# Optimization experiments

Hardware: AMD Instinct MI355X
Metric: run time of the kernel (lower is better)

## Reference

```python
import jax, jax.numpy as jnp
import numpy as np

B, Z, H, TC, TD, DOUT = 128, 512, 512, 16, 16, 176
DIN_DEC = DOUT + H  # 688: concat(prev_note, conductor_embedding)


def setup_inputs() -> dict:
    key = jax.random.key(0)
    ks = jax.random.split(key, 24)

    def glorot(k, shape):
        lim = np.sqrt(6.0 / (shape[0] + shape[1]))
        return jax.random.uniform(k, shape, jnp.float32, -lim, lim)

    return {
        'z_ssm_embedding': jax.random.normal(ks[0], (B, Z), jnp.float32),
        'pianoroll': jax.random.uniform(ks[1], (B, TC * TD, DOUT), jnp.float32),
        'ssm': jax.random.uniform(ks[2], (B, TC * TD, TC * TD), jnp.float32),
        # z -> conductor initial states (h1,c1,h2,c2), tanh dense
        'Wz': glorot(ks[3], (Z, 4 * H)), 'bz': jnp.zeros((4 * H,), jnp.float32),
        # conductor 2-layer LSTM (input 512)
        'cond_W1': glorot(ks[4], (H, 4 * H)), 'cond_U1': glorot(ks[5], (H, 4 * H)), 'cond_b1': jnp.zeros((4 * H,), jnp.float32),
        'cond_W2': glorot(ks[6], (H, 4 * H)), 'cond_U2': glorot(ks[7], (H, 4 * H)), 'cond_b2': jnp.zeros((4 * H,), jnp.float32),
        # conductor embedding -> decoder initial states, tanh dense
        'Wcd': glorot(ks[8], (H, 4 * H)), 'bcd': jnp.zeros((4 * H,), jnp.float32),
        # core decoder 2-layer LSTM (input 688)
        'dec_W1': glorot(ks[9], (DIN_DEC, 4 * H)), 'dec_U1': glorot(ks[10], (H, 4 * H)), 'dec_b1': jnp.zeros((4 * H,), jnp.float32),
        'dec_W2': glorot(ks[11], (H, 4 * H)), 'dec_U2': glorot(ks[12], (H, 4 * H)), 'dec_b2': jnp.zeros((4 * H,), jnp.float32),
        # output projection (softmax)
        'Wp': glorot(ks[13], (H, DOUT)), 'bp': jnp.zeros((DOUT,), jnp.float32),
    }


def _lstm_step(x, h, c, W, U, b):
    g = x @ W + h @ U + b  # (B, 4H), keras gate order i,f,g,o
    i, f, gg, o = jnp.split(g, 4, axis=-1)
    c = jax.nn.sigmoid(f) * c + jax.nn.sigmoid(i) * jnp.tanh(gg)
    h = jax.nn.sigmoid(o) * jnp.tanh(c)
    return h, c


def reference(z_ssm_embedding, pianoroll, ssm,
              Wz, bz,
              cond_W1, cond_U1, cond_b1, cond_W2, cond_U2, cond_b2,
              Wcd, bcd,
              dec_W1, dec_U1, dec_b1, dec_W2, dec_U2, dec_b2,
              Wp, bp):
    b = z_ssm_embedding.shape[0]
    # conductor initial states from latent (tanh dense, split per layer h/c)
    s = jnp.tanh(z_ssm_embedding @ Wz + bz)
    ch1, cc1, ch2, cc2 = jnp.split(s, 4, axis=-1)
    # In the source, conductor_input and conductor_states are never updated
    # across the outer loop, so the conductor embedding is identical for all
    # 16 segments: compute the single step once.
    x0 = jnp.zeros((b, H), jnp.float32)
    h1, _ = _lstm_step(x0, ch1, cc1, cond_W1, cond_U1, cond_b1)
    cond_emb, _ = _lstm_step(h1, ch2, cc2, cond_W2, cond_U2, cond_b2)  # (B, H)
    # decoder initial states from conductor embedding (same for all segments)
    sd = jnp.tanh(cond_emb @ Wcd + bcd)
    dh1, dc1, dh2, dc2 = jnp.split(sd, 4, axis=-1)

    def seg(note_prev, _):
        def step(carry, _):
            h1, c1, h2, c2, note = carry
            x = jnp.concatenate([note, cond_emb], axis=-1)  # (B, 688)
            h1, c1 = _lstm_step(x, h1, c1, dec_W1, dec_U1, dec_b1)
            h2, c2 = _lstm_step(h1, h2, c2, dec_W2, dec_U2, dec_b2)
            note = jax.nn.softmax(h2 @ Wp + bp, axis=-1)  # output projection
            return (h1, c1, h2, c2, note), note
        (_, _, _, _, note_last), notes = jax.lax.scan(
            step, (dh1, dc1, dh2, dc2, note_prev), None, length=TD)
        return note_last, notes  # notes: (TD, B, DOUT)

    note0 = jnp.zeros((b, DOUT), jnp.float32)
    _, all_notes = jax.lax.scan(seg, note0, None, length=TC)  # (TC, TD, B, DOUT)
    return all_notes.reshape(TC * TD, b, DOUT).transpose(1, 0, 2)  # (B, 256, 176)
```

## Files before the change

kernel.cpp:

```cpp
#include <hip/hip_runtime.h>
#include <hip/hip_bf16.h>
#include <math.h>

#define Bn    128
#define NGn   2048
#define TTn   256
#define DOn   176
#define NBLK  256
#define NTHR  1024
#define HPAR  65536
#define ACC_PAR 24576

typedef unsigned int uint;
using f32x4 = __attribute__((ext_vector_type(4))) float;
using s16x8 = __attribute__((ext_vector_type(8))) short;
union FR { uint u[4]; s16x8 s; };

struct KA {
  const float *z,*Wz,*bz,*cU1,*cb1,*cW2,*cU2,*cb2,*Wcd,*bcd;
  const float *dW1,*dU1,*db1,*dW2,*dU2,*db2,*Wp,*bp;
  float *zT,*sT,*ggate,*h1cT,*ceT,*sdT,*beffP,*db1P,*db2P,*WEp,*out;
  uint *WAh,*WAl,*WBh,*WBl,*h1pk,*h2pk,*dh1pk,*dh2pk;
  int  *accI;
};

__device__ unsigned g_cnt_l1[16 * 32];
__device__ unsigned g_cnt;
__device__ unsigned g_gen;
__device__ unsigned pod_ctr[8 * 64];

__device__ __forceinline__ float sigm(float x) { return 1.0f / (1.0f + __expf(-x)); }

__device__ __forceinline__ float aloadF(const float* p) {
  return __hip_atomic_load(p, __ATOMIC_RELAXED, __HIP_MEMORY_SCOPE_AGENT);
}
__device__ __forceinline__ void astoreF(float* p, float v) {
  __hip_atomic_store(p, v, __ATOMIC_RELAXED, __HIP_MEMORY_SCOPE_AGENT);
}
__device__ __forceinline__ uint aloadU(const uint* p) {
  return __hip_atomic_load(p, __ATOMIC_RELAXED, __HIP_MEMORY_SCOPE_AGENT);
}
__device__ __forceinline__ void astoreU(uint* p, uint v) {
  __hip_atomic_store(p, v, __ATOMIC_RELAXED, __HIP_MEMORY_SCOPE_AGENT);
}
__device__ __forceinline__ int aloadI(const int* p) {
  return __hip_atomic_load(p, __ATOMIC_RELAXED, __HIP_MEMORY_SCOPE_AGENT);
}

__device__ __forceinline__ void split2(float v, unsigned short& h, unsigned short& l) {
  __hip_bfloat16 bh = __float2bfloat16(v);
  float hf = __bfloat162float(bh);
  __hip_bfloat16 bl = __float2bfloat16(v - hf);
  h = *(unsigned short*)&bh; l = *(unsigned short*)&bl;
}
__device__ __forceinline__ uint packsplit(float v) {
  unsigned short h, l; split2(v, h, l);
  return (uint)h | ((uint)l << 16);
}

__device__ __forceinline__ void gbar() {
  __syncthreads();
  if (threadIdx.x == 0) {
    asm volatile("s_waitcnt vmcnt(0)" ::: "memory");
    unsigned g0 = __hip_atomic_load(&g_gen, __ATOMIC_RELAXED, __HIP_MEMORY_SCOPE_AGENT);
    unsigned p1 = __hip_atomic_fetch_add(&g_cnt_l1[(blockIdx.x >> 4) * 32], 1u,
                                         __ATOMIC_RELAXED, __HIP_MEMORY_SCOPE_AGENT);
    if (p1 == 15u) {
      unsigned p2 = __hip_atomic_fetch_add(&g_cnt, 1u, __ATOMIC_RELAXED, __HIP_MEMORY_SCOPE_AGENT);
      if (p2 == 15u) {
        #pragma unroll
        for (int i = 0; i < 16; i++)
          __hip_atomic_store(&g_cnt_l1[i * 32], 0u, __ATOMIC_RELAXED, __HIP_MEMORY_SCOPE_AGENT);
        __hip_atomic_store(&g_cnt, 0u, __ATOMIC_RELAXED, __HIP_MEMORY_SCOPE_AGENT);
        asm volatile("s_waitcnt vmcnt(0)" ::: "memory");
        __hip_atomic_fetch_add(&g_gen, 1u, __ATOMIC_RELAXED, __HIP_MEMORY_SCOPE_AGENT);
      }
    }
    while (__hip_atomic_load(&g_gen, __ATOMIC_RELAXED, __HIP_MEMORY_SCOPE_AGENT) == g0)
      __builtin_amdgcn_s_sleep(1);
  }
  __syncthreads();
}

__device__ __forceinline__ void pbar2(int pod, unsigned& tgt) {
  __syncthreads();
  if (threadIdx.x == 0) {
    asm volatile("s_waitcnt vmcnt(0)" ::: "memory");
    unsigned* ctr = &pod_ctr[pod * 64];
    __hip_atomic_fetch_add(ctr, 1u, __ATOMIC_RELAXED, __HIP_MEMORY_SCOPE_AGENT);
    while ((int)(__hip_atomic_load(ctr, __ATOMIC_RELAXED, __HIP_MEMORY_SCOPE_AGENT) - tgt) < 0) { }
  }
  __syncthreads();
  tgt += 32;
}

__device__ __forceinline__ void stageN(float* __restrict__ xs, const float* __restrict__ X,
                                       int nrows, int b0, int tid) {
  for (int i = tid; i < nrows * 16; i += NTHR)
    xs[i] = aloadF(X + (size_t)(i >> 4) * Bn + b0 + (i & 15));
}

template<int KC>
__device__ __forceinline__ void gemm16(const float* __restrict__ Wb, int colbase,
                                       int kq, int cg, int bg,
                                       const float* __restrict__ xsrc, float acc[16]) {
  const float* wp = Wb + (size_t)(kq * KC) * NGn + colbase + cg * 4;
  const float* xp = xsrc + (kq * KC) * 16 + bg * 4;
  #pragma unroll 2
  for (int kk = 0; kk < KC; kk++) {
    const float4 w4 = *(const float4*)(wp);
    const float4 x4 = *(const float4*)(xp);
    acc[0]  = fmaf(w4.x, x4.x, acc[0]);  acc[1]  = fmaf(w4.x, x4.y, acc[1]);
    acc[2]  = fmaf(w4.x, x4.z, acc[2]);  acc[3]  = fmaf(w4.x, x4.w, acc[3]);
    acc[4]  = fmaf(w4.y, x4.x, acc[4]);  acc[5]  = fmaf(w4.y, x4.y, acc[5]);
    acc[6]  = fmaf(w4.y, x4.z, acc[6]);  acc[7]  = fmaf(w4.y, x4.w, acc[7]);
    acc[8]  = fmaf(w4.z, x4.x, acc[8]);  acc[9]  = fmaf(w4.z, x4.y, acc[9]);
    acc[10] = fmaf(w4.z, x4.z, acc[10]); acc[11] = fmaf(w4.z, x4.w, acc[11]);
    acc[12] = fmaf(w4.w, x4.x, acc[12]); acc[13] = fmaf(w4.w, x4.y, acc[13]);
    acc[14] = fmaf(w4.w, x4.z, acc[14]); acc[15] = fmaf(w4.w, x4.w, acc[15]);
    wp += NGn; xp += 16;
  }
}

__device__ __forceinline__ void pstore(float* __restrict__ part, int kq, int cg, int bg,
                                       const float acc[16]) {
  #pragma unroll
  for (int c = 0; c < 4; c++) {
    float* p = part + (size_t)(kq * 64 + cg * 4 + c) * 17 + bg * 4;
    *(float4*)p = make_float4(acc[c*4], acc[c*4+1], acc[c*4+2], acc[c*4+3]);
  }
}

template<int MODE>
__device__ __forceinline__ void epi_plain(const float* bias, float* out,
                                          int colbase, int b0, int tid,
                                          const float* __restrict__ part) {
  int cl = tid >> 4, bl = tid & 15;
  float s = 0.0f;
  #pragma unroll
  for (int w = 0; w < 8; w++) s += part[(w * 64 + cl) * 17 + bl];
  if (bias) s += bias[colbase + cl];
  if (MODE == 0) s = tanhf(s);
  astoreF(out + (size_t)(colbase + cl) * Bn + b0 + bl, s);
}

__device__ __forceinline__ void cond_nl(const float* gb, const float* cbias,
                                        const float* cin, float* hout, int bid, int tid) {
  int i = bid * NTHR + tid;
  if (i < 512 * Bn) {
    int hid = i >> 7, b = i & 127;
    float gi = aloadF(gb + (size_t)hid * Bn + b)            + cbias[hid];
    float gf = aloadF(gb + (size_t)(512 + hid) * Bn + b)    + cbias[512 + hid];
    float gg = aloadF(gb + (size_t)(1024 + hid) * Bn + b)   + cbias[1024 + hid];
    float go = aloadF(gb + (size_t)(1536 + hid) * Bn + b)   + cbias[1536 + hid];
    float cprev = aloadF(cin + (size_t)hid * Bn + b);
    float c = sigm(gf) * cprev + sigm(gi) * tanhf(gg);
    astoreF(hout + (size_t)hid * Bn + b, sigm(go) * tanhf(c));
  }
}

__device__ __forceinline__ void ldxK(const uint* __restrict__ base, FR& xh, FR& xl) {
  uint w[8];
  #pragma unroll
  for (int e = 0; e < 8; e++) w[e] = aloadU(base + e * 128);
  xh.u[0] = (w[0] & 0xffffu) | (w[1] << 16); xl.u[0] = (w[0] >> 16) | (w[1] & 0xffff0000u);
  xh.u[1] = (w[2] & 0xffffu) | (w[3] << 16); xl.u[1] = (w[2] >> 16) | (w[3] & 0xffff0000u);
  xh.u[2] = (w[4] & 0xffffu) | (w[5] << 16); xl.u[2] = (w[4] >> 16) | (w[5] & 0xffff0000u);
  xh.u[3] = (w[6] & 0xffffu) | (w[7] << 16); xl.u[3] = (w[6] >> 16) | (w[7] & 0xffff0000u);
}
__device__ __forceinline__ void ldxL17(const uint* __restrict__ p, FR& xh, FR& xl) {
  uint w[8];
  #pragma unroll
  for (int e = 0; e < 8; e++) w[e] = p[e * 17];
  xh.u[0] = (w[0] & 0xffffu) | (w[1] << 16); xl.u[0] = (w[0] >> 16) | (w[1] & 0xffff0000u);
  xh.u[1] = (w[2] & 0xffffu) | (w[3] << 16); xl.u[1] = (w[2] >> 16) | (w[3] & 0xffff0000u);
  xh.u[2] = (w[4] & 0xffffu) | (w[5] << 16); xl.u[2] = (w[4] >> 16) | (w[5] & 0xffff0000u);
  xh.u[3] = (w[6] & 0xffffu) | (w[7] << 16); xl.u[3] = (w[6] >> 16) | (w[7] & 0xffff0000u);
}

struct MC {
  const uint *WAh,*WAl,*WBh,*WBl,*dh1pk,*dh2pk;
  uint *h1pk,*h2pk;
  const float *beffP,*db2P,*Wp,*bp;
  int *accI;
  float *out;
  uint *NTu;
  float *plog,*gbuf,*cst,*h2s;
  int j, b0;
};

#define MFMA3(ACC, XH, XL, WH, WL)                                            \
  ACC = __builtin_amdgcn_mfma_f32_16x16x32_bf16(XH.s, WH.s, ACC, 0, 0, 0);    \
  ACC = __builtin_amdgcn_mfma_f32_16x16x32_bf16(XL.s, WH.s, ACC, 0, 0, 0);    \
  ACC = __builtin_amdgcn_mfma_f32_16x16x32_bf16(XH.s, WL.s, ACC, 0, 0, 0);

__device__ __forceinline__ void phaseA(const MC& c, int t, bool doLSTM) {
  const int tid = threadIdx.x, wid = tid >> 6, lane = tid & 63;
  const int m = lane & 15, kh = lane >> 4;
  const int par = t & 1; const bool rst = (t & 15) == 0;
  if (t > 0) {
    const int wv = wid;
    const int* ai = c.accI + ((par ^ 1) * ACC_PAR) + wv * 192;
    float lg[3], pv[3];
    #pragma unroll
    for (int rep = 0; rep < 3; rep++) {
      int o = lane + rep * 64;
      lg[rep] = (o < DOn) ? (float)aloadI(ai + o) * (1.0f / 1048576.0f) + c.bp[o] : -1e30f;
    }
    float mx = fmaxf(fmaxf(lg[0], lg[1]), lg[2]);
    #pragma unroll
    for (int d = 1; d < 64; d <<= 1) mx = fmaxf(mx, __shfl_xor(mx, d));
    float sum = 0.f;
    #pragma unroll
    for (int rep = 0; rep < 3; rep++) {
      int o = lane + rep * 64;
      pv[rep] = (o < DOn) ? __expf(lg[rep] - mx) : 0.f;
      sum += pv[rep];
    }
    #pragma unroll
    for (int d = 1; d < 64; d <<= 1) sum += __shfl_xor(sum, d);
    const float inv = 1.0f / sum;
    #pragma unroll
    for (int rep = 0; rep < 3; rep++) {
      int o = lane + rep * 64;
      float p = pv[rep] * inv;
      c.NTu[o * 17 + wv] = (o < DOn) ? packsplit(p) : 0u;
      if (c.j < 16 && wv == c.j && o < DOn)
        c.out[((size_t)(c.b0 + c.j) * TTn + (t - 1)) * DOn + o] = p;
    }
  }
  __syncthreads();
  if (!doLSTM) return;
  const int nt = wid & 3, ksq = wid >> 2;
  const int s0 = (ksq == 0) ? 0 : (ksq == 1) ? 6 : (ksq == 2) ? 12 : 17;
  const int s1 = (ksq == 0) ? 6 : (ksq == 1) ? 12 : (ksq == 2) ? 17 : 22;
  const uint* hb = (rst ? c.dh1pk : (c.h1pk + (par ^ 1) * HPAR)) + kh * 8 * 128 + c.b0 + m;
  f32x4 acc = {0.f,0.f,0.f,0.f};
  for (int ks = s0; ks < s1; ks++) {
    FR xh, xl;
    if (ks < 6) ldxL17(c.NTu + (ks * 32 + kh * 8) * 17 + m, xh, xl);
    else        ldxK(hb + (ks * 32 - 192) * 128, xh, xl);
    FR wh, wl;
    *(uint4*)wh.u = *(const uint4*)(c.WAh + (size_t)c.j * 22528 + (ks * 4 + nt) * 256 + lane * 4);
    *(uint4*)wl.u = *(const uint4*)(c.WAl + (size_t)c.j * 22528 + (ks * 4 + nt) * 256 + lane * 4);
    MFMA3(acc, xh, xl, wh, wl)
  }
  #pragma unroll
  for (int r = 0; r < 4; r++) c.plog[((ksq * 4 + nt) * 4 + r) * 64 + lane] = acc[r];
  __syncthreads();
  {
    int cl = tid >> 4, bl = tid & 15;
    float s = 0.f;
    #pragma unroll
    for (int k2 = 0; k2 < 4; k2++)
      s += c.plog[((k2 * 4 + (cl >> 4)) * 4 + (bl & 3)) * 64 + (bl >> 2) * 16 + (cl & 15)];
    c.gbuf[cl * 16 + bl] = s + c.beffP[(size_t)(c.j * 64 + cl) * Bn + c.b0 + bl];
  }
  __syncthreads();
  if (tid < 256) {
    int h = tid >> 4, bl = tid & 15;
    float gi = c.gbuf[(h*4+0)*16+bl], gf = c.gbuf[(h*4+1)*16+bl];
    float gg = c.gbuf[(h*4+2)*16+bl], go = c.gbuf[(h*4+3)*16+bl];
    float cp = rst ? c.cst[512 + tid] : c.cst[tid];
    float cc = sigm(gf) * cp + sigm(gi) * tanhf(gg);
    c.cst[tid] = cc;
    astoreU(c.h1pk + par * HPAR + (size_t)(c.j * 16 + h) * 128 + c.b0 + bl,
            packsplit(sigm(go) * tanhf(cc)));
  }
}

__device__ __forceinline__ void phaseB(const MC& c, int t) {
  const int tid = threadIdx.x, wid = tid >> 6, lane = tid & 63;
  const int m = lane & 15, kh = lane >> 4;
  const int nt = wid & 3, ksq = wid >> 2;
  const int par = t & 1; const bool rst = (t & 15) == 0;
  const uint* s1b = c.h1pk + par * HPAR + kh * 8 * 128 + c.b0 + m;
  const uint* s2b = (rst ? c.dh2pk : (c.h2pk + (par ^ 1) * HPAR)) + kh * 8 * 128 + c.b0 + m;
  f32x4 acc = {0.f,0.f,0.f,0.f};
  #pragma unroll
  for (int kk = 0; kk < 8; kk++) {
    const int ks = ksq * 8 + kk;
    FR xh, xl;
    if (ksq < 2) ldxK(s1b + ks * 32 * 128, xh, xl);
    else         ldxK(s2b + (ks - 16) * 32 * 128, xh, xl);
    FR wh, wl;
    *(uint4*)wh.u = *(const uint4*)(c.WBh + (size_t)c.j * 32768 + (ks * 4 + nt) * 256 + lane * 4);
    *(uint4*)wl.u = *(const uint4*)(c.WBl + (size_t)c.j * 32768 + (ks * 4 + nt) * 256 + lane * 4);
    MFMA3(acc, xh, xl, wh, wl)
  }
  #pragma unroll
  for (int r = 0; r < 4; r++) c.plog[((ksq * 4 + nt) * 4 + r) * 64 + lane] = acc[r];
  __syncthreads();
  {
    int cl = tid >> 4, bl = tid & 15;
    float s = 0.f;
    #pragma unroll
    for (int k2 = 0; k2 < 4; k2++)
      s += c.plog[((k2 * 4 + (cl >> 4)) * 4 + (bl & 3)) * 64 + (bl >> 2) * 16 + (cl & 15)];
    c.gbuf[cl * 16 + bl] = s + c.db2P[c.j * 64 + cl];
  }
  __syncthreads();
  if (tid < 256) {
    int h = tid >> 4, bl = tid & 15;
    float gi = c.gbuf[(h*4+0)*16+bl], gf = c.gbuf[(h*4+1)*16+bl];
    float gg = c.gbuf[(h*4+2)*16+bl], go = c.gbuf[(h*4+3)*16+bl];
    float cp = rst ? c.cst[768 + tid] : c.cst[256 + tid];
    float cc = sigm(gf) * cp + sigm(gi) * tanhf(gg);
    c.cst[256 + tid] = cc;
    float h2v = sigm(go) * tanhf(cc);
    c.h2s[h * 16 + bl] = h2v;
    astoreU(c.h2pk + par * HPAR + (size_t)(c.j * 16 + h) * 128 + c.b0 + bl, packsplit(h2v));
  }
  __syncthreads();
  const int o = tid & 255, q = tid >> 8;
  if (o < DOn) {
    float wv[16];
    #pragma unroll
    for (int h = 0; h < 16; h++) wv[h] = c.Wp[(size_t)(c.j * 16 + h) * DOn + o];
    #pragma unroll
    for (int rep = 0; rep < 4; rep++) {
      const int bl = q * 4 + rep;
      float s = 0.f;
      #pragma unroll
      for (int h = 0; h < 16; h++) s = fmaf(c.h2s[h * 16 + bl], wv[h], s);
      __hip_atomic_fetch_add(c.accI + par * ACC_PAR + bl * 192 + o,
                             __float2int_rn(s * 1048576.0f),
                             __ATOMIC_RELAXED, __HIP_MEMORY_SCOPE_AGENT);
    }
  }
  if (tid < 96)
    astoreU((uint*)(c.accI + (par ^ 1) * ACC_PAR + c.j * 96 + tid), 0u);
}

__global__ void __launch_bounds__(NTHR, 1)
hd_kernel(KA A) {
  __shared__ float buf[25088];
  float* xs = buf;
  float* part = buf + 16384;
  const int bid = blockIdx.x, tid = threadIdx.x;
  const int lane = tid & 63;
  const int kqP = tid >> 6, cgP = lane & 15, bgP = lane >> 4;
  const int rP = bid & 31, btP = bid >> 5;
  const int htP = (rP & 7) * 4 + (rP >> 3);
  const int colbaseP = htP * 64, b0P = btP * 16;
  const int pod = bid >> 5;

  unsigned tgt = __hip_atomic_load(&pod_ctr[pod * 64], __ATOMIC_RELAXED,
                                   __HIP_MEMORY_SCOPE_AGENT) + 32;

  {
    const int i0 = bid * NTHR + tid;
    if (i0 < 512 * Bn) { int zb = i0 >> 9, zk = i0 & 511; astoreF(A.zT + (size_t)zk * Bn + zb, A.z[i0]); }
    if (i0 < NGn) {
      int hid = i0 >> 2, g = i0 & 3, sc = g * 512 + hid;
      astoreF(A.db1P + i0, A.db1[sc]);
      astoreF(A.db2P + i0, A.db2[sc]);
    }
    if (i0 < 2 * ACC_PAR) astoreU((uint*)(A.accI + i0), 0u);
    for (int i = i0; i < 512 * NGn; i += NBLK * NTHR) {
      int k = i >> 11, pc = i & 2047;
      int hid = pc >> 2, g = pc & 3;
      astoreF(A.WEp + i, A.dW1[(size_t)(176 + k) * NGn + g * 512 + hid]);
    }
    for (int i = i0; i < 720896; i += NBLK * NTHR) {
      int col = i & 2047, kp = i >> 11, k = kp * 2;
      float w0, w1;
      if (k < 176)      { w0 = A.dW1[(size_t)k * NGn + col];       w1 = A.dW1[(size_t)(k + 1) * NGn + col]; }
      else if (k < 192) { w0 = 0.f; w1 = 0.f; }
      else              { w0 = A.dU1[(size_t)(k - 192) * NGn + col]; w1 = A.dU1[(size_t)(k - 191) * NGn + col]; }
      unsigned short h0, l0, h1, l1; split2(w0, h0, l0); split2(w1, h1, l1);
      int g = col >> 9, hid = col & 511;
      int jj = hid >> 4, cl = (hid & 15) * 4 + g;
      int nt = cl >> 4, n = cl & 15;
      int ks = k >> 5, kr = k & 31, lh = kr >> 3, q = (kr >> 1) & 3;
      int idx = ((jj * 22 + ks) * 4 + nt) * 256 + (lh * 16 + n) * 4 + q;
      astoreU(A.WAh + idx, (uint)h0 | ((uint)h1 << 16));
      astoreU(A.WAl + idx, (uint)l0 | ((uint)l1 << 16));
    }
  }
  gbar();
  {
    stageN(xs, A.zT, 512, b0P, tid); __syncthreads();
    if (tid < 512) {
      float acc[16] = {0,0,0,0,0,0,0,0,0,0,0,0,0,0,0,0};
      gemm16<64>(A.Wz, colbaseP, kqP, cgP, bgP, xs, acc);
      pstore(part, kqP, cgP, bgP, acc);
    }
    __syncthreads();
    epi_plain<0>(A.bz, A.sT, colbaseP, b0P, tid, part);
  }
  gbar();
  {
    stageN(xs, A.sT, 512, b0P, tid); __syncthreads();
    if (tid < 512) {
      float acc[16] = {0,0,0,0,0,0,0,0,0,0,0,0,0,0,0,0};
      gemm16<64>(A.cU1, colbaseP, kqP, cgP, bgP, xs, acc);
      pstore(part, kqP, cgP, bgP, acc);
    }
    __syncthreads();
    epi_plain<1>(nullptr, A.ggate, colbaseP, b0P, tid, part);
  }
  gbar();
  cond_nl(A.ggate, A.cb1, A.sT + (size_t)512 * Bn, A.h1cT, bid, tid);
  gbar();
  {
    stageN(xs, A.h1cT, 512, b0P, tid);
    stageN(xs + 8192, A.sT + (size_t)1024 * Bn, 512, b0P, tid);
    __syncthreads();
    if (tid < 512) {
      float acc[16] = {0,0,0,0,0,0,0,0,0,0,0,0,0,0,0,0};
      gemm16<64>(A.cW2, colbaseP, kqP, cgP, bgP, xs, acc);
      gemm16<64>(A.cU2, colbaseP, kqP, cgP, bgP, xs + 8192, acc);
      pstore(part, kqP, cgP, bgP, acc);
    }
    __syncthreads();
    epi_plain<1>(nullptr, A.ggate, colbaseP, b0P, tid, part);
  }
  gbar();
  cond_nl(A.ggate, A.cb2, A.sT + (size_t)1536 * Bn, A.ceT, bid, tid);
  gbar();
  {
    stageN(xs, A.ceT, 512, b0P, tid); __syncthreads();
    if (tid < 512) {
      float acc[16] = {0,0,0,0,0,0,0,0,0,0,0,0,0,0,0,0};
      gemm16<64>(A.Wcd, colbaseP, kqP, cgP, bgP, xs, acc);
      pstore(part, kqP, cgP, bgP, acc);
    }
    __syncthreads();
    epi_plain<0>(A.bcd, A.sdT, colbaseP, b0P, tid, part);
    __syncthreads();
    if (tid < 512) {
      float acc[16] = {0,0,0,0,0,0,0,0,0,0,0,0,0,0,0,0};
      gemm16<64>(A.WEp, colbaseP, kqP, cgP, bgP, xs, acc);
      pstore(part, kqP, cgP, bgP, acc);
    }
    __syncthreads();
    epi_plain<1>(A.db1P, A.beffP, colbaseP, b0P, tid, part);
  }
  gbar();
  {
    const int i0 = bid * NTHR + tid;
    for (int i = i0; i < 1048576; i += NBLK * NTHR) {
      int col = i & 2047, kp = i >> 11, k = kp * 2;
      float w0, w1;
      if (k < 512) { w0 = A.dW2[(size_t)k * NGn + col];         w1 = A.dW2[(size_t)(k + 1) * NGn + col]; }
      else         { w0 = A.dU2[(size_t)(k - 512) * NGn + col]; w1 = A.dU2[(size_t)(k - 511) * NGn + col]; }
      unsigned short h0, l0, h1, l1; split2(w0, h0, l0); split2(w1, h1, l1);
      int g = col >> 9, hid = col & 511;
      int jj = hid >> 4, cl = (hid & 15) * 4 + g;
      int nt = cl >> 4, n = cl & 15;
      int ks = k >> 5, kr = k & 31, lh = kr >> 3, q = (kr >> 1) & 3;
      int idx = ((jj * 32 + ks) * 4 + nt) * 256 + (lh * 16 + n) * 4 + q;
      astoreU(A.WBh + idx, (uint)h0 | ((uint)h1 << 16));
      astoreU(A.WBl + idx, (uint)l0 | ((uint)l1 << 16));
    }
    if (i0 < 512 * Bn) {
      int hid = i0 >> 7, b = i0 & 127;
      astoreU(A.dh1pk + hid * 128 + b, packsplit(aloadF(A.sdT + (size_t)hid * Bn + b)));
      astoreU(A.dh2pk + hid * 128 + b, packsplit(aloadF(A.sdT + (size_t)(1024 + hid) * Bn + b)));
    }
  }
  gbar();

  MC c;
  c.WAh = A.WAh; c.WAl = A.WAl; c.WBh = A.WBh; c.WBl = A.WBl;
  c.dh1pk = A.dh1pk; c.dh2pk = A.dh2pk;
  c.h1pk = A.h1pk; c.h2pk = A.h2pk;
  c.beffP = A.beffP; c.db2P = A.db2P; c.Wp = A.Wp; c.bp = A.bp; c.out = A.out;
  c.accI = A.accI + pod * 3072;
  c.NTu = (uint*)buf;
  c.plog = buf + 3264;
  c.gbuf = buf + 7360;
  c.cst  = buf + 8384;
  c.h2s  = buf + 9408;
  c.j = bid & 31;
  c.b0 = pod * 16;
  if (tid < 256) {
    int h = tid >> 4, bl = tid & 15;
    c.cst[512 + tid] = aloadF(A.sdT + (size_t)(512 + c.j * 16 + h) * Bn + c.b0 + bl);
    c.cst[768 + tid] = aloadF(A.sdT + (size_t)(1536 + c.j * 16 + h) * Bn + c.b0 + bl);
  }
  for (int i = tid; i < 3264; i += NTHR) c.NTu[i] = 0u;
  __syncthreads();

  for (int t = 0; t < TTn; t++) {
    phaseA(c, t, true);
    pbar2(pod, tgt);
    phaseB(c, t);
    pbar2(pod, tgt);
  }
  phaseA(c, TTn, false);
}

extern "C" void kernel_launch(void* const* d_in, const int* in_sizes, int n_in,
                              void* d_out, int out_size, void* d_ws, size_t ws_size,
                              hipStream_t stream) {
  (void)in_sizes; (void)n_in; (void)out_size; (void)ws_size;
  KA a;
  a.z   = (const float*)d_in[0];
  a.Wz  = (const float*)d_in[3];  a.bz  = (const float*)d_in[4];
  a.cU1 = (const float*)d_in[6];  a.cb1 = (const float*)d_in[7];
  a.cW2 = (const float*)d_in[8];  a.cU2 = (const float*)d_in[9];  a.cb2 = (const float*)d_in[10];
  a.Wcd = (const float*)d_in[11]; a.bcd = (const float*)d_in[12];
  a.dW1 = (const float*)d_in[13]; a.dU1 = (const float*)d_in[14]; a.db1 = (const float*)d_in[15];
  a.dW2 = (const float*)d_in[16]; a.dU2 = (const float*)d_in[17]; a.db2 = (const float*)d_in[18];
  a.Wp  = (const float*)d_in[19]; a.bp  = (const float*)d_in[20];

  float* ws = (float*)d_ws;
  size_t off = 0;
  a.zT    = ws + off; off += (size_t)512  * Bn;
  a.sT    = ws + off; off += (size_t)NGn  * Bn;
  a.ggate = ws + off; off += (size_t)NGn  * Bn;
  a.h1cT  = ws + off; off += (size_t)512  * Bn;
  a.ceT   = ws + off; off += (size_t)512  * Bn;
  a.sdT   = ws + off; off += (size_t)NGn  * Bn;
  a.beffP = ws + off; off += (size_t)NGn  * Bn;
  a.db1P  = ws + off; off += (size_t)NGn;
  a.db2P  = ws + off; off += (size_t)NGn;
  a.WEp   = ws + off; off += (size_t)512 * NGn;
  a.WBh   = (uint*)a.WEp;
  a.WBl   = (uint*)(ws + off); off += (size_t)1048576;
  a.WAh   = (uint*)(ws + off); off += (size_t)720896;
  a.WAl   = (uint*)(ws + off); off += (size_t)720896;
  a.h1pk  = (uint*)(ws + off); off += (size_t)2 * HPAR;
  a.h2pk  = (uint*)(ws + off); off += (size_t)2 * HPAR;
  a.dh1pk = (uint*)(ws + off); off += (size_t)HPAR;
  a.dh2pk = (uint*)(ws + off); off += (size_t)HPAR;
  a.accI  = (int*)(ws + off);  off += (size_t)2 * ACC_PAR;
  a.out   = (float*)d_out;

  hd_kernel<<<dim3(NBLK), dim3(NTHR), 0, stream>>>(a);
}
```

Before: 7.773 ms.

## Repack hidden states for 64-bit loads and split K across all waves

Changes the packed h1/h2/note layout so each lane fetches eight consecutive k values with four 64-bit (or two 128-bit LDS) loads instead of eight strided 32-bit loads. Work is redistributed so each wave owns one or two K-slices across all four N-tiles, and a 16-way LDS reduction with padded stride replaces the previous 4-way split. Per-step bias values are cached in shared memory instead of reread from global memory. This trades more LDS traffic and registers in the reduction for fewer, wider global loads on the latency-bound recurrent critical path.

```diff
diff --git a/kernel.cpp b/kernel.cpp
--- a/kernel.cpp
+++ b/kernel.cpp
@@ -12,6 +12,7 @@
 #define ACC_PAR 24576
 
 typedef unsigned int uint;
+typedef unsigned long long u64;
 using f32x4 = __attribute__((ext_vector_type(4))) float;
 using s16x8 = __attribute__((ext_vector_type(8))) short;
 union FR { uint u[4]; s16x8 s; };
@@ -44,6 +45,9 @@
   __hip_atomic_store(p, v, __ATOMIC_RELAXED, __HIP_MEMORY_SCOPE_AGENT);
 }
 __device__ __forceinline__ int aloadI(const int* p) {
+  return __hip_atomic_load(p, __ATOMIC_RELAXED, __HIP_MEMORY_SCOPE_AGENT);
+}
+__device__ __forceinline__ u64 aload64(const u64* p) {
   return __hip_atomic_load(p, __ATOMIC_RELAXED, __HIP_MEMORY_SCOPE_AGENT);
 }
 
@@ -159,23 +163,19 @@
   }
 }
 
-__device__ __forceinline__ void ldxK(const uint* __restrict__ base, FR& xh, FR& xl) {
-  uint w[8];
-  #pragma unroll
-  for (int e = 0; e < 8; e++) w[e] = aloadU(base + e * 128);
-  xh.u[0] = (w[0] & 0xffffu) | (w[1] << 16); xl.u[0] = (w[0] >> 16) | (w[1] & 0xffff0000u);
-  xh.u[1] = (w[2] & 0xffffu) | (w[3] << 16); xl.u[1] = (w[2] >> 16) | (w[3] & 0xffff0000u);
-  xh.u[2] = (w[4] & 0xffffu) | (w[5] << 16); xl.u[2] = (w[4] >> 16) | (w[5] & 0xffff0000u);
-  xh.u[3] = (w[6] & 0xffffu) | (w[7] << 16); xl.u[3] = (w[6] >> 16) | (w[7] & 0xffff0000u);
-}
-__device__ __forceinline__ void ldxL17(const uint* __restrict__ p, FR& xh, FR& xl) {
-  uint w[8];
-  #pragma unroll
-  for (int e = 0; e < 8; e++) w[e] = p[e * 17];
-  xh.u[0] = (w[0] & 0xffffu) | (w[1] << 16); xl.u[0] = (w[0] >> 16) | (w[1] & 0xffff0000u);
-  xh.u[1] = (w[2] & 0xffffu) | (w[3] << 16); xl.u[1] = (w[2] >> 16) | (w[3] & 0xffff0000u);
-  xh.u[2] = (w[4] & 0xffffu) | (w[5] << 16); xl.u[2] = (w[4] >> 16) | (w[5] & 0xffff0000u);
-  xh.u[3] = (w[6] & 0xffffu) | (w[7] << 16); xl.u[3] = (w[6] >> 16) | (w[7] & 0xffff0000u);
+__device__ __forceinline__ void unpack64(const u64* d, FR& xh, FR& xl) {
+  #pragma unroll
+  for (int q = 0; q < 4; q++) {
+    uint lo = (uint)d[q], hi = (uint)(d[q] >> 32);
+    xh.u[q] = (lo & 0xffffu) | (hi << 16);
+    xl.u[q] = (lo >> 16) | (hi & 0xffff0000u);
+  }
+}
+__device__ __forceinline__ void unpackU8(uint4 a, uint4 b, FR& xh, FR& xl) {
+  xh.u[0] = (a.x & 0xffffu) | (a.y << 16); xl.u[0] = (a.x >> 16) | (a.y & 0xffff0000u);
+  xh.u[1] = (a.z & 0xffffu) | (a.w << 16); xl.u[1] = (a.z >> 16) | (a.w & 0xffff0000u);
+  xh.u[2] = (b.x & 0xffffu) | (b.y << 16); xl.u[2] = (b.x >> 16) | (b.y & 0xffff0000u);
+  xh.u[3] = (b.z & 0xffffu) | (b.w << 16); xl.u[3] = (b.z >> 16) | (b.w & 0xffff0000u);
 }
 
 struct MC {
@@ -194,7 +194,36 @@
   ACC = __builtin_amdgcn_mfma_f32_16x16x32_bf16(XL.s, WH.s, ACC, 0, 0, 0);    \
   ACC = __builtin_amdgcn_mfma_f32_16x16x32_bf16(XH.s, WL.s, ACC, 0, 0, 0);
 
-__device__ __forceinline__ void phaseA(const MC& c, int t, bool doLSTM) {
+__device__ __forceinline__ void doKS(const uint* WH, const uint* WL, int ks, int lane,
+                                     const FR& xh, const FR& xl, f32x4 acc[4]) {
+  #pragma unroll
+  for (int nt = 0; nt < 4; nt++) {
+    FR wh, wl;
+    *(uint4*)wh.u = *(const uint4*)(WH + (ks * 4 + nt) * 256 + lane * 4);
+    *(uint4*)wl.u = *(const uint4*)(WL + (ks * 4 + nt) * 256 + lane * 4);
+    MFMA3(acc[nt], xh, xl, wh, wl)
+  }
+}
+
+__device__ __forceinline__ void wrplog(const MC& c, int wid, int lane, const f32x4 acc[4]) {
+  #pragma unroll
+  for (int nt = 0; nt < 4; nt++)
+    #pragma unroll
+    for (int r = 0; r < 4; r++)
+      c.plog[((wid * 4 + nt) * 4 + r) * 68 + lane] = acc[nt][r];
+}
+
+__device__ __forceinline__ void reduce16(const MC& c, int tid, const float* biasv) {
+  int cl = tid >> 4, bl = tid & 15;
+  float s = 0.f;
+  #pragma unroll
+  for (int k2 = 0; k2 < 16; k2++)
+    s += c.plog[((k2 * 4 + (cl >> 4)) * 4 + (bl & 3)) * 68 + (bl >> 2) * 16 + (cl & 15)];
+  c.gbuf[cl * 16 + bl] = s + biasv[cl * 16 + bl];
+}
+
+__device__ __forceinline__ void phaseA(const MC& c, int t, bool doLSTM,
+                                       float* __restrict__ beffL) {
   const int tid = threadIdx.x, wid = tid >> 6, lane = tid & 63;
   const int m = lane & 15, kh = lane >> 4;
   const int par = t & 1; const bool rst = (t & 15) == 0;
@@ -224,38 +253,51 @@
     for (int rep = 0; rep < 3; rep++) {
       int o = lane + rep * 64;
       float p = pv[rep] * inv;
-      c.NTu[o * 17 + wv] = (o < DOn) ? packsplit(p) : 0u;
+      c.NTu[((o >> 3) * 16 + wv) * 8 + (o & 7)] = (o < DOn) ? packsplit(p) : 0u;
       if (c.j < 16 && wv == c.j && o < DOn)
         c.out[((size_t)(c.b0 + c.j) * TTn + (t - 1)) * DOn + o] = p;
     }
   }
   __syncthreads();
   if (!doLSTM) return;
-  const int nt = wid & 3, ksq = wid >> 2;
-  const int s0 = (ksq == 0) ? 0 : (ksq == 1) ? 6 : (ksq == 2) ? 12 : 17;
-  const int s1 = (ksq == 0) ? 6 : (ksq == 1) ? 12 : (ksq == 2) ? 17 : 22;
-  const uint* hb = (rst ? c.dh1pk : (c.h1pk + (par ^ 1) * HPAR)) + kh * 8 * 128 + c.b0 + m;
-  f32x4 acc = {0.f,0.f,0.f,0.f};
-  for (int ks = s0; ks < s1; ks++) {
-    FR xh, xl;
-    if (ks < 6) ldxL17(c.NTu + (ks * 32 + kh * 8) * 17 + m, xh, xl);
-    else        ldxK(hb + (ks * 32 - 192) * 128, xh, xl);
-    FR wh, wl;
-    *(uint4*)wh.u = *(const uint4*)(c.WAh + (size_t)c.j * 22528 + (ks * 4 + nt) * 256 + lane * 4);
-    *(uint4*)wl.u = *(const uint4*)(c.WAl + (size_t)c.j * 22528 + (ks * 4 + nt) * 256 + lane * 4);
-    MFMA3(acc, xh, xl, wh, wl)
-  }
-  #pragma unroll
-  for (int r = 0; r < 4; r++) c.plog[((ksq * 4 + nt) * 4 + r) * 64 + lane] = acc[r];
-  __syncthreads();
-  {
-    int cl = tid >> 4, bl = tid & 15;
-    float s = 0.f;
-    #pragma unroll
-    for (int k2 = 0; k2 < 4; k2++)
-      s += c.plog[((k2 * 4 + (cl >> 4)) * 4 + (bl & 3)) * 64 + (bl >> 2) * 16 + (cl & 15)];
-    c.gbuf[cl * 16 + bl] = s + c.beffP[(size_t)(c.j * 64 + cl) * Bn + c.b0 + bl];
-  }
+  const uint* WH = c.WAh + (size_t)c.j * 22528;
+  const uint* WL = c.WAl + (size_t)c.j * 22528;
+  const uint* hsrc = rst ? c.dh1pk : (c.h1pk + (par ^ 1) * HPAR);
+  f32x4 acc[4] = {{0,0,0,0},{0,0,0,0},{0,0,0,0},{0,0,0,0}};
+  if (wid < 3) {
+    #pragma unroll
+    for (int i = 0; i < 2; i++) {
+      const int ks = wid * 2 + i;
+      const uint* p = c.NTu + ((ks * 4 + kh) * 16 + m) * 8;
+      uint4 a = *(const uint4*)p, b = *(const uint4*)(p + 4);
+      FR xh, xl; unpackU8(a, b, xh, xl);
+      doKS(WH, WL, ks, lane, xh, xl, acc);
+    }
+  } else if (wid < 6) {
+    u64 xr[8];
+    #pragma unroll
+    for (int i = 0; i < 2; i++) {
+      const int ks = wid * 2 + i;
+      const u64* p = (const u64*)hsrc + ((size_t)(((ks - 6) * 4 + kh) * 128 + c.b0 + m)) * 4;
+      #pragma unroll
+      for (int q = 0; q < 4; q++) xr[i * 4 + q] = aload64(p + q);
+    }
+    #pragma unroll
+    for (int i = 0; i < 2; i++) {
+      FR xh, xl; unpack64(&xr[i * 4], xh, xl);
+      doKS(WH, WL, wid * 2 + i, lane, xh, xl, acc);
+    }
+  } else {
+    u64 xr[4];
+    const u64* p = (const u64*)hsrc + ((size_t)((wid * 4 + kh) * 128 + c.b0 + m)) * 4;
+    #pragma unroll
+    for (int q = 0; q < 4; q++) xr[q] = aload64(p + q);
+    FR xh, xl; unpack64(xr, xh, xl);
+    doKS(WH, WL, 12 + (wid - 6), lane, xh, xl, acc);
+  }
+  wrplog(c, wid, lane, acc);
+  __syncthreads();
+  reduce16(c, tid, beffL);
   __syncthreads();
   if (tid < 256) {
     int h = tid >> 4, bl = tid & 15;
@@ -264,41 +306,38 @@
     float cp = rst ? c.cst[512 + tid] : c.cst[tid];
     float cc = sigm(gf) * cp + sigm(gi) * tanhf(gg);
     c.cst[tid] = cc;
-    astoreU(c.h1pk + par * HPAR + (size_t)(c.j * 16 + h) * 128 + c.b0 + bl,
+    astoreU(c.h1pk + par * HPAR
+              + ((size_t)((c.j * 2 + (h >> 3)) * 128 + c.b0 + bl)) * 8 + (h & 7),
             packsplit(sigm(go) * tanhf(cc)));
   }
 }
 
-__device__ __forceinline__ void phaseB(const MC& c, int t) {
+__device__ __forceinline__ void phaseB(const MC& c, int t, float* __restrict__ db2L) {
   const int tid = threadIdx.x, wid = tid >> 6, lane = tid & 63;
   const int m = lane & 15, kh = lane >> 4;
-  const int nt = wid & 3, ksq = wid >> 2;
   const int par = t & 1; const bool rst = (t & 15) == 0;
-  const uint* s1b = c.h1pk + par * HPAR + kh * 8 * 128 + c.b0 + m;
-  const uint* s2b = (rst ? c.dh2pk : (c.h2pk + (par ^ 1) * HPAR)) + kh * 8 * 128 + c.b0 + m;
-  f32x4 acc = {0.f,0.f,0.f,0.f};
-  #pragma unroll
-  for (int kk = 0; kk < 8; kk++) {
-    const int ks = ksq * 8 + kk;
-    FR xh, xl;
-    if (ksq < 2) ldxK(s1b + ks * 32 * 128, xh, xl);
-    else         ldxK(s2b + (ks - 16) * 32 * 128, xh, xl);
-    FR wh, wl;
-    *(uint4*)wh.u = *(const uint4*)(c.WBh + (size_t)c.j * 32768 + (ks * 4 + nt) * 256 + lane * 4);
-    *(uint4*)wl.u = *(const uint4*)(c.WBl + (size_t)c.j * 32768 + (ks * 4 + nt) * 256 + lane * 4);
-    MFMA3(acc, xh, xl, wh, wl)
-  }
-  #pragma unroll
-  for (int r = 0; r < 4; r++) c.plog[((ksq * 4 + nt) * 4 + r) * 64 + lane] = acc[r];
-  __syncthreads();
-  {
-    int cl = tid >> 4, bl = tid & 15;
-    float s = 0.f;
-    #pragma unroll
-    for (int k2 = 0; k2 < 4; k2++)
-      s += c.plog[((k2 * 4 + (cl >> 4)) * 4 + (bl & 3)) * 64 + (bl >> 2) * 16 + (cl & 15)];
-    c.gbuf[cl * 16 + bl] = s + c.db2P[c.j * 64 + cl];
-  }
+  const uint* s1 = c.h1pk + par * HPAR;
+  const uint* s2 = rst ? c.dh2pk : (c.h2pk + (par ^ 1) * HPAR);
+  const uint* WH = c.WBh + (size_t)c.j * 32768;
+  const uint* WL = c.WBl + (size_t)c.j * 32768;
+  u64 xr[8];
+  #pragma unroll
+  for (int i = 0; i < 2; i++) {
+    const int ks = wid * 2 + i;
+    const uint* sp = (ks < 16) ? s1 : s2;
+    const u64* p = (const u64*)sp + ((size_t)(((ks & 15) * 4 + kh) * 128 + c.b0 + m)) * 4;
+    #pragma unroll
+    for (int q = 0; q < 4; q++) xr[i * 4 + q] = aload64(p + q);
+  }
+  f32x4 acc[4] = {{0,0,0,0},{0,0,0,0},{0,0,0,0},{0,0,0,0}};
+  #pragma unroll
+  for (int i = 0; i < 2; i++) {
+    FR xh, xl; unpack64(&xr[i * 4], xh, xl);
+    doKS(WH, WL, wid * 2 + i, lane, xh, xl, acc);
+  }
+  wrplog(c, wid, lane, acc);
+  __syncthreads();
+  reduce16(c, tid, db2L);
   __syncthreads();
   if (tid < 256) {
     int h = tid >> 4, bl = tid & 15;
@@ -309,7 +348,9 @@
     c.cst[256 + tid] = cc;
     float h2v = sigm(go) * tanhf(cc);
     c.h2s[h * 16 + bl] = h2v;
-    astoreU(c.h2pk + par * HPAR + (size_t)(c.j * 16 + h) * 128 + c.b0 + bl, packsplit(h2v));
+    astoreU(c.h2pk + par * HPAR
+              + ((size_t)((c.j * 2 + (h >> 3)) * 128 + c.b0 + bl)) * 8 + (h & 7),
+            packsplit(h2v));
   }
   __syncthreads();
   const int o = tid & 255, q = tid >> 8;
@@ -335,6 +376,7 @@
 __global__ void __launch_bounds__(NTHR, 1)
 hd_kernel(KA A) {
   __shared__ float buf[25088];
+  __shared__ float beffL[1024], db2L[1024];
   float* xs = buf;
   float* part = buf + 16384;
   const int bid = blockIdx.x, tid = threadIdx.x;
@@ -456,8 +498,10 @@
     }
     if (i0 < 512 * Bn) {
       int hid = i0 >> 7, b = i0 & 127;
-      astoreU(A.dh1pk + hid * 128 + b, packsplit(aloadF(A.sdT + (size_t)hid * Bn + b)));
-      astoreU(A.dh2pk + hid * 128 + b, packsplit(aloadF(A.sdT + (size_t)(1024 + hid) * Bn + b)));
+      astoreU(A.dh1pk + ((size_t)((hid >> 3) * 128 + b)) * 8 + (hid & 7),
+              packsplit(aloadF(A.sdT + (size_t)hid * Bn + b)));
+      astoreU(A.dh2pk + ((size_t)((hid >> 3) * 128 + b)) * 8 + (hid & 7),
+              packsplit(aloadF(A.sdT + (size_t)(1024 + hid) * Bn + b)));
     }
   }
   gbar();
@@ -469,10 +513,10 @@
   c.beffP = A.beffP; c.db2P = A.db2P; c.Wp = A.Wp; c.bp = A.bp; c.out = A.out;
   c.accI = A.accI + pod * 3072;
   c.NTu = (uint*)buf;
-  c.plog = buf + 3264;
-  c.gbuf = buf + 7360;
-  c.cst  = buf + 8384;
-  c.h2s  = buf + 9408;
+  c.plog = buf + 3072;
+  c.gbuf = buf + 20480;
+  c.cst  = buf + 21504;
+  c.h2s  = buf + 22528;
   c.j = bid & 31;
   c.b0 = pod * 16;
   if (tid < 256) {
@@ -480,16 +524,21 @@
     c.cst[512 + tid] = aloadF(A.sdT + (size_t)(512 + c.j * 16 + h) * Bn + c.b0 + bl);
     c.cst[768 + tid] = aloadF(A.sdT + (size_t)(1536 + c.j * 16 + h) * Bn + c.b0 + bl);
   }
-  for (int i = tid; i < 3264; i += NTHR) c.NTu[i] = 0u;
+  {
+    int cl = tid >> 4, bl = tid & 15;
+    beffL[tid] = aloadF(A.beffP + (size_t)(c.j * 64 + cl) * Bn + c.b0 + bl);
+    db2L[tid] = A.db2P[c.j * 64 + cl];
+  }
+  for (int i = tid; i < 3072; i += NTHR) c.NTu[i] = 0u;
   __syncthreads();
 
   for (int t = 0; t < TTn; t++) {
-    phaseA(c, t, true);
+    phaseA(c, t, true, beffL);
     pbar2(pod, tgt);
-    phaseB(c, t);
+    phaseB(c, t, db2L);
     pbar2(pod, tgt);
   }
-  phaseA(c, TTn, false);
+  phaseA(c, TTn, false, beffL);
 }
 
 extern "C" void kernel_launch(void* const* d_in, const int* in_sizes, int n_in,
```

Result: faster. 7.156 ms (-7.9%).
